# Performance work log

Measured on AMD Instinct MI355X. Metric: run time of the kernel, lower is better.

The kernel has to match this reference:

```python
import jax, jax.numpy as jnp
import numpy as np
from jax import lax

GRID_N = 80
C_FEAT = 128
HID = 256
NLAYERS = 12


def _make_grid_mesh(n):
    xs = np.linspace(-0.9, 0.9, n, dtype=np.float32)
    X, Y = np.meshgrid(xs, xs, indexing='xy')
    verts = np.stack([X.ravel(), Y.ravel(), np.zeros(n * n, np.float32)], 1)
    idx = np.arange(n * n).reshape(n, n)
    a = idx[:-1, :-1].ravel(); b = idx[:-1, 1:].ravel()
    c = idx[1:, :-1].ravel(); d = idx[1:, 1:].ravel()
    faces = np.concatenate([np.stack([a, b, c], 1), np.stack([b, d, c], 1)], 0)
    return verts, faces.astype(np.int64)


def _edges_and_inv(faces):
    F = faces.shape[0]
    e = np.concatenate([faces[:, [0, 1]], faces[:, [1, 2]], faces[:, [2, 0]]], 0)
    e = np.sort(e, 1)
    edges, inv = np.unique(e, axis=0, return_inverse=True)
    inv = inv.reshape(-1)
    return edges.astype(np.int32), inv[:F], inv[F:2 * F], inv[2 * F:]


def _subdivide_faces(faces, V):
    # new vertex k is midpoint of unique edge k, placed at index V + k
    edges, i01, i12, i20 = _edges_and_inv(faces)
    m01 = V + i01; m12 = V + i12; m20 = V + i20
    v0, v1, v2 = faces[:, 0], faces[:, 1], faces[:, 2]
    nf = np.concatenate([np.stack([v0, m01, m20], 1), np.stack([v1, m12, m01], 1),
                         np.stack([v2, m20, m12], 1), np.stack([m01, m12, m20], 1)], 0)
    return edges, nf


def _topology():
    verts0, f1 = _make_grid_mesh(GRID_N)
    V1 = verts0.shape[0]
    edges1, f2 = _subdivide_faces(f1, V1)
    V2 = V1 + edges1.shape[0]
    edges2, f3 = _subdivide_faces(f2, V2)
    V3 = V2 + edges2.shape[0]
    edges3 = _edges_and_inv(f3)[0]
    return verts0, edges1, edges2, edges3, V3


def _vert_align(feat, verts):
    # feat [C,H,W]; sample bilinearly at vertex (x,y) in [-1,1], align_corners, zero padding
    C, H, W = feat.shape
    fx = (verts[:, 0] + 1.0) * 0.5 * (W - 1)
    fy = (verts[:, 1] + 1.0) * 0.5 * (H - 1)
    x0 = jnp.floor(fx); y0 = jnp.floor(fy)
    wx = fx - x0; wy = fy - y0
    x0i = x0.astype(jnp.int32); y0i = y0.astype(jnp.int32)
    fT = jnp.transpose(feat, (1, 2, 0))  # [H,W,C]

    def samp(yi, xi):
        valid = ((yi >= 0) & (yi < H) & (xi >= 0) & (xi < W)).astype(feat.dtype)
        v = fT[jnp.clip(yi, 0, H - 1), jnp.clip(xi, 0, W - 1)]
        return v * valid[:, None]

    return (samp(y0i, x0i) * ((1 - wy) * (1 - wx))[:, None]
            + samp(y0i, x0i + 1) * ((1 - wy) * wx)[:, None]
            + samp(y0i + 1, x0i) * (wy * (1 - wx))[:, None]
            + samp(y0i + 1, x0i + 1) * (wy * wx)[:, None])


def _gconv(x, e0, e1, w, b):
    # pytorch3d GraphConv: w0(x) + sum_{j in N(i)} w1(x_j), undirected edges
    h0 = x @ w[0] + b[0]
    h1 = x @ w[1] + b[1]
    agg = jnp.zeros_like(h0).at[e0].add(h1[e1]).at[e1].add(h1[e0])
    return h0 + agg


def _stage(feat, edges, w_in, b_in, w_h, b_h, w_out, b_out):
    e0, e1 = edges[:, 0], edges[:, 1]
    x = _gconv(feat, e0, e1, w_in, b_in)

    def body(xc, p):
        return _gconv(xc, e0, e1, p[0], p[1]), None

    x, _ = lax.scan(body, x, (w_h, b_h))
    coords = _gconv(x, e0, e1, w_out, b_out)
    return x, coords


def _subdiv(f, edges):
    # SubdivideMeshes feature/vertex rule: append edge midpoints
    return jnp.concatenate([f, 0.5 * (f[edges[:, 0]] + f[edges[:, 1]])], 0)


def setup_inputs() -> dict:
    key = jax.random.key(0)
    ks = jax.random.split(key, 16)
    verts0, edges1, edges2, edges3, V3 = _topology()

    def pw(k, din, dout, L=None):
        shape = (L, 2, din, dout) if L else (2, din, dout)
        return jax.random.normal(k, shape, dtype=jnp.float32) / np.float32(np.sqrt(7.0 * din))

    din2 = C_FEAT + HID
    inp = {
        'conv64': jax.random.normal(ks[0], (C_FEAT, 56, 56), jnp.float32),
        'conv128': jax.random.normal(ks[1], (C_FEAT, 28, 28), jnp.float32),
        'conv256': jax.random.normal(ks[2], (C_FEAT, 14, 14), jnp.float32),
        'verts0': jnp.asarray(verts0),
        'edges1': jnp.asarray(edges1), 'edges2': jnp.asarray(edges2), 'edges3': jnp.asarray(edges3),
        'w_in1': pw(ks[3], C_FEAT, HID), 'b_in1': jnp.zeros((2, HID), jnp.float32),
        'w_h1': pw(ks[4], HID, HID, NLAYERS), 'b_h1': jnp.zeros((NLAYERS, 2, HID), jnp.float32),
        'w_out1': pw(ks[5], HID, 3), 'b_out1': jnp.zeros((2, 3), jnp.float32),
        'w_in2': pw(ks[6], din2, HID), 'b_in2': jnp.zeros((2, HID), jnp.float32),
        'w_h2': pw(ks[7], HID, HID, NLAYERS), 'b_h2': jnp.zeros((NLAYERS, 2, HID), jnp.float32),
        'w_out2': pw(ks[8], HID, 3), 'b_out2': jnp.zeros((2, 3), jnp.float32),
        'w_in3': pw(ks[9], din2, HID), 'b_in3': jnp.zeros((2, HID), jnp.float32),
        'w_h3': pw(ks[10], HID, HID, NLAYERS), 'b_h3': jnp.zeros((NLAYERS, 2, HID), jnp.float32),
        'w_out3': pw(ks[11], HID, 3), 'b_out3': jnp.zeros((2, 3), jnp.float32),
    }
    return inp


def reference(conv64, conv128, conv256, verts0,
              w_in1, b_in1, w_h1, b_h1, w_out1, b_out1,
              w_in2, b_in2, w_h2, b_h2, w_out2, b_out2,
              w_in3, b_in3, w_h3, b_h3, w_out3, b_out3,
              edges1, edges2, edges3):
    # stage 1: vert_align on conv64 + 14 graph convs -> coords
    x, c1 = _stage(_vert_align(conv64, verts0), edges1, w_in1, b_in1, w_h1, b_h1, w_out1, b_out1)
    v2 = _subdiv(c1, edges1)
    h2 = _subdiv(x, edges1)
    f2 = jnp.concatenate([_vert_align(conv128, v2), h2], 1)
    x, c2 = _stage(f2, edges2, w_in2, b_in2, w_h2, b_h2, w_out2, b_out2)
    v3 = _subdiv(c2, edges2)
    h3 = _subdiv(x, edges2)
    f3 = jnp.concatenate([_vert_align(conv256, v3), h3], 1)
    _, c3 = _stage(f3, edges3, w_in3, b_in3, w_h3, b_h3, w_out3, b_out3)
    return c3
```

## Files before the change

kernel.cpp:

```cpp
#include <hip/hip_runtime.h>
#include <utility>

#define HID 256

typedef __attribute__((ext_vector_type(8))) short bf16x8;
typedef __attribute__((ext_vector_type(4))) float f32x4;
typedef __attribute__((ext_vector_type(4))) unsigned short us4;
typedef __attribute__((ext_vector_type(8))) unsigned short us8;

constexpr size_t MAXN3 = 100489;
constexpr size_t MAXE3 = 300200;

constexpr size_t OFF_IN1 = 0;
constexpr size_t OFF_IN2 = OFF_IN1 + 2 * 256 * 128;
constexpr size_t OFF_IN3 = OFF_IN2 + 2 * 256 * 384;
constexpr size_t OFF_H1  = OFF_IN3 + 2 * 256 * 384;
constexpr size_t OFF_H2  = OFF_H1 + 24 * 256 * 256;
constexpr size_t OFF_H3  = OFF_H2 + 24 * 256 * 256;
constexpr size_t WT_TOTAL = OFF_H3 + 24 * 256 * 256;

__device__ __attribute__((aligned(16))) unsigned short g_Ah[MAXN3 * 256];
__device__ __attribute__((aligned(16))) unsigned short g_Al[MAXN3 * 256];
__device__ __attribute__((aligned(16))) unsigned short g_Bh[MAXN3 * 256];
__device__ __attribute__((aligned(16))) unsigned short g_Bl[MAXN3 * 256];
__device__ __attribute__((aligned(16))) unsigned short g_Gh[MAXN3 * 256];
__device__ __attribute__((aligned(16))) unsigned short g_Gl[MAXN3 * 256];
__device__ __attribute__((aligned(16))) unsigned short g_Dh[MAXN3 * 256];
__device__ __attribute__((aligned(16))) unsigned short g_Dl[MAXN3 * 256];
__device__ __attribute__((aligned(16))) unsigned short g_VAh[MAXN3 * 128];
__device__ __attribute__((aligned(16))) unsigned short g_VAl[MAXN3 * 128];
__device__ float g_C0[MAXN3 * 3];
__device__ float g_C2[MAXN3 * 3];
__device__ float g_Vv[MAXN3 * 3];
__device__ float g_T [56 * 56 * 128];
__device__ __attribute__((aligned(16))) unsigned short g_Wth[WT_TOTAL];
__device__ __attribute__((aligned(16))) unsigned short g_Wtl[WT_TOTAL];
__device__ int g_deg   [MAXN3];
__device__ int g_rowptr[MAXN3 + 1];
__device__ int g_cursor[MAXN3];
__device__ int g_adj   [2 * MAXE3];
__device__ int g_bsum  [128];

__device__ inline float b2f(unsigned short h) {
  return __uint_as_float((unsigned)h << 16);
}
__device__ inline void fsplit(float f, unsigned short& h, unsigned short& l) {
  unsigned u = __float_as_uint(f);
  h = (unsigned short)(u >> 16);
  float hf = __uint_as_float(u & 0xffff0000u);
  l = (unsigned short)(__float_as_uint(f - hf) >> 16);
}

#define GLOAD16(g, l)                                                       \
  __builtin_amdgcn_global_load_lds(                                        \
      (const __attribute__((address_space(1))) unsigned*)(const void*)(g), \
      (__attribute__((address_space(3))) unsigned*)(void*)(l), 16, 0, 0)

__global__ __launch_bounds__(256) void k_wtrans(const float* __restrict__ W,
                                                unsigned short* __restrict__ Oh,
                                                unsigned short* __restrict__ Ol,
                                                int K) {
  __shared__ float Ls[64][65];
  int ktb = blockIdx.x, cb = blockIdx.y, mat = blockIdx.z;
  int nktb = gridDim.x;
  const float* Wm = W + (size_t)mat * K * 256;
  int t = threadIdx.x;
#pragma unroll
  for (int i = 0; i < 16; ++i) {
    int idx = i * 256 + t;
    int kk = idx >> 6, cc = idx & 63;
    Ls[kk][cc] = Wm[(size_t)(ktb * 64 + kk) * 256 + cb * 64 + cc];
  }
  __syncthreads();
  size_t tb = ((size_t)(mat * 4 + cb) * nktb + ktb) * 4096;
#pragma unroll
  for (int i = 0; i < 2; ++i) {
    int c = t * 2 + i;
    int n = c >> 3, sp = c & 7;
    int kbase = (sp ^ (n & 7)) * 8;
    unsigned short hb[8], lb[8];
#pragma unroll
    for (int j = 0; j < 8; ++j) {
      float v = Ls[kbase + j][n];
      unsigned short hi, lo;
      fsplit(v, hi, lo);
      hb[j] = hi;
      lb[j] = lo;
    }
    *(us4*)(Oh + tb + c * 8)     = (us4){hb[0], hb[1], hb[2], hb[3]};
    *(us4*)(Oh + tb + c * 8 + 4) = (us4){hb[4], hb[5], hb[6], hb[7]};
    *(us4*)(Ol + tb + c * 8)     = (us4){lb[0], lb[1], lb[2], lb[3]};
    *(us4*)(Ol + tb + c * 8 + 4) = (us4){lb[4], lb[5], lb[6], lb[7]};
  }
}


__global__ __launch_bounds__(256) void k_count(const int* __restrict__ edges,
                                               int* __restrict__ deg, int E) {
  int e = blockIdx.x * blockDim.x + threadIdx.x;
  if (e >= E) return;
  atomicAdd(&deg[edges[2 * e + 0]], 1);
  atomicAdd(&deg[edges[2 * e + 1]], 1);
}

__global__ __launch_bounds__(256) void k_scan_part(const int* __restrict__ deg,
                                                   int* __restrict__ bsum, int N) {
  __shared__ int s[256];
  int t = threadIdx.x;
  int base = blockIdx.x * 1024 + t * 4;
  int v = 0;
#pragma unroll
  for (int i = 0; i < 4; ++i) {
    int idx = base + i;
    if (idx < N) v += deg[idx];
  }
  s[t] = v;
  __syncthreads();
  for (int off = 128; off > 0; off >>= 1) {
    if (t < off) s[t] += s[t + off];
    __syncthreads();
  }
  if (t == 0) bsum[blockIdx.x] = s[0];
}

__global__ __launch_bounds__(128) void k_scan_top(int* __restrict__ bsum, int nb) {
  __shared__ int s[128];
  int t = threadIdx.x;
  s[t] = (t < nb) ? bsum[t] : 0;
  __syncthreads();
  for (int off = 1; off < 128; off <<= 1) {
    int v = (t >= off) ? s[t - off] : 0;
    __syncthreads();
    s[t] += v;
    __syncthreads();
  }
  if (t < nb) bsum[t] = (t == 0) ? 0 : s[t - 1];
}

__global__ __launch_bounds__(256) void k_scan_write(const int* __restrict__ deg,
                                                    const int* __restrict__ bsum,
                                                    int* __restrict__ rowptr,
                                                    int* __restrict__ cursor, int N) {
  __shared__ int s[256];
  int t = threadIdx.x;
  int base = blockIdx.x * 1024;
  int d[4];
  int local = 0;
#pragma unroll
  for (int i = 0; i < 4; ++i) {
    int idx = base + t * 4 + i;
    d[i] = (idx < N) ? deg[idx] : 0;
    local += d[i];
  }
  s[t] = local;
  __syncthreads();
  for (int off = 1; off < 256; off <<= 1) {
    int v = (t >= off) ? s[t - off] : 0;
    __syncthreads();
    s[t] += v;
    __syncthreads();
  }
  int run = bsum[blockIdx.x] + s[t] - local;
#pragma unroll
  for (int i = 0; i < 4; ++i) {
    int idx = base + t * 4 + i;
    if (idx < N) {
      rowptr[idx] = run;
      cursor[idx] = run;
    }
    run += d[i];
  }
  if (blockIdx.x == gridDim.x - 1 && t == 255) rowptr[N] = run;
}

__global__ __launch_bounds__(256) void k_fill(const int* __restrict__ edges,
                                              int* __restrict__ cursor,
                                              int* __restrict__ adj, int E) {
  int e = blockIdx.x * blockDim.x + threadIdx.x;
  if (e >= E) return;
  int a = edges[2 * e + 0];
  int b = edges[2 * e + 1];
  adj[atomicAdd(&cursor[a], 1)] = b;
  adj[atomicAdd(&cursor[b], 1)] = a;
}


__global__ __launch_bounds__(128) void k_transpose(const float* __restrict__ in,
                                                   float* __restrict__ out, int HW) {
  int p = blockIdx.x;
  int c = threadIdx.x;
  if (p < HW) out[(size_t)p * 128 + c] = in[(size_t)c * HW + p];
}

__global__ __launch_bounds__(128) void k_vert_align(const float* __restrict__ fT,
                                                    const float* __restrict__ verts,
                                                    unsigned short* __restrict__ oh,
                                                    unsigned short* __restrict__ ol,
                                                    int N, int H, int W) {
  int v = blockIdx.x;
  if (v >= N) return;
  int c = threadIdx.x;
  float vx = verts[(size_t)v * 3 + 0];
  float vy = verts[(size_t)v * 3 + 1];
  float fx = (vx + 1.f) * 0.5f * (float)(W - 1);
  float fy = (vy + 1.f) * 0.5f * (float)(H - 1);
  float x0f = floorf(fx), y0f = floorf(fy);
  float wx = fx - x0f, wy = fy - y0f;
  int x0 = (int)x0f, y0 = (int)y0f;
  float acc = 0.f;
#pragma unroll
  for (int dy = 0; dy < 2; ++dy) {
#pragma unroll
    for (int dx = 0; dx < 2; ++dx) {
      int yi = y0 + dy, xi = x0 + dx;
      bool valid = (yi >= 0) && (yi < H) && (xi >= 0) && (xi < W);
      int yc = min(max(yi, 0), H - 1);
      int xc = min(max(xi, 0), W - 1);
      float val = fT[((size_t)yc * W + xc) * 128 + c];
      float wgt = (dy ? wy : 1.f - wy) * (dx ? wx : 1.f - wx);
      acc += valid ? val * wgt : 0.f;
    }
  }
  unsigned short h, l;
  fsplit(acc, h, l);
  oh[(size_t)v * 128 + c] = h;
  ol[(size_t)v * 128 + c] = l;
}

template <int CH>
__global__ __launch_bounds__(256) void k_gather(const int* __restrict__ rowptr,
                                                const int* __restrict__ adj,
                                                const unsigned short* __restrict__ Xh,
                                                const unsigned short* __restrict__ Xl,
                                                unsigned short* __restrict__ Gh,
                                                unsigned short* __restrict__ Gl, int N) {
  constexpr int TPV = CH / 8;
  int idx = blockIdx.x * blockDim.x + threadIdx.x;
  int v = idx / TPV;
  if (v >= N) return;
  int c = (idx % TPV) * 8;
  float a[8] = {};
  int lo = rowptr[v], hi = rowptr[v + 1];
  for (int i = lo; i < hi; ++i) {
    size_t base = (size_t)adj[i] * CH + c;
    us8 h = *(const us8*)(Xh + base);
    us8 l = *(const us8*)(Xl + base);
#pragma unroll
    for (int j = 0; j < 8; ++j) a[j] += b2f(h[j]) + b2f(l[j]);
  }
  us8 oh, ol;
#pragma unroll
  for (int j = 0; j < 8; ++j) {
    unsigned short hh, ll;
    fsplit(a[j], hh, ll);
    oh[j] = hh;
    ol[j] = ll;
  }
  *(us8*)(Gh + (size_t)v * CH + c) = oh;
  *(us8*)(Gl + (size_t)v * CH + c) = ol;
}

struct Panels {
  const unsigned short* ph[4];
  const unsigned short* pl[4];
  int ks[4];
  int ld[4];
};

#define SWZ(row, slot) (((row) * 64) + (((slot) ^ ((row) & 7)) << 3))

__global__ __launch_bounds__(512, 2) void k_layer(
    Panels pd, int Kmm,
    const unsigned short* __restrict__ w0h, const unsigned short* __restrict__ w0l,
    const unsigned short* __restrict__ w1h, const unsigned short* __restrict__ w1l,
    int Kw,
    const float* __restrict__ b0, const float* __restrict__ b1,
    const int* __restrict__ deg,
    unsigned short* __restrict__ Yh, unsigned short* __restrict__ Yl, int N) {
  __shared__ __attribute__((aligned(16))) unsigned short Xh_lds[2][128 * 64];
  __shared__ __attribute__((aligned(16))) unsigned short Xl_lds[2][128 * 64];
  __shared__ __attribute__((aligned(16))) unsigned short Wh_lds[2][2 * 4096];
  __shared__ __attribute__((aligned(16))) unsigned short Wl_lds[2][2 * 4096];
  int tid = threadIdx.x;
  int lane = tid & 63;
  int wid = tid >> 6;
  int wm = wid >> 2;
  int wn = wid & 3;

  int nrt = (N + 127) >> 7;
  int total = nrt * 2;
  int flat = blockIdx.x;
  int rowtile, colblk;
  if ((flat & ~15) + 16 <= total) {
    int sub = flat & 15;
    rowtile = (flat >> 4) * 8 + (sub & 7);
    colblk = sub >> 3;
  } else {
    rowtile = flat >> 1;
    colblk = flat & 1;
  }
  int row0 = rowtile * 128;
  int col0 = colblk * 128;
  int nktbw = Kw >> 6;

  f32x4 acc[4][2];
#pragma unroll
  for (int m = 0; m < 4; ++m)
#pragma unroll
    for (int n = 0; n < 2; ++n) acc[m][n] = (f32x4){0.f, 0.f, 0.f, 0.f};

  auto STAGE = [&](int buf, int kt) {
    int pi = (kt >= pd.ks[1]) + (kt >= pd.ks[2]) + (kt >= pd.ks[3]);
    const unsigned short* bph = pd.ph[pi];
    const unsigned short* bpl = pd.pl[pi];
    int ld = pd.ld[pi];
    int koff = kt - pd.ks[pi];
#pragma unroll
    for (int i = 0; i < 2; ++i) {
      int c = tid + i * 512;
      int row = c >> 3, slot = c & 7;
      int vg = min(row0 + row, N - 1);
      size_t so = (size_t)vg * ld + koff + ((slot ^ (row & 7)) << 3);
      GLOAD16(bph + so, &Xh_lds[buf][(size_t)c * 8]);
      GLOAD16(bpl + so, &Xl_lds[buf][(size_t)c * 8]);
    }
    int ktb = (kt < Kw) ? (kt >> 6) : ((kt - Kw) >> 6);
    const unsigned short* mh = (kt < Kw) ? w0h : w1h;
    const unsigned short* ml = (kt < Kw) ? w0l : w1l;
#pragma unroll
    for (int i = 0; i < 2; ++i) {
      int c = tid + i * 512;
      int half = c >> 9, ci = c & 511;
      size_t tb = ((size_t)((2 * colblk + half) * nktbw + ktb)) * 4096 + (size_t)ci * 8;
      GLOAD16(mh + tb, &Wh_lds[buf][half * 4096 + ci * 8]);
      GLOAD16(ml + tb, &Wl_lds[buf][half * 4096 + ci * 8]);
    }
  };

  auto COMPUTE = [&](int buf) {
#pragma unroll
    for (int ks = 0; ks < 2; ++ks) {
      int slot = ks * 4 + (lane >> 4);
      bf16x8 ah[4], al[4];
#pragma unroll
      for (int m = 0; m < 4; ++m) {
        int row = wm * 64 + m * 16 + (lane & 15);
        int off = SWZ(row, slot);
        ah[m] = *(const bf16x8*)&Xh_lds[buf][off];
        al[m] = *(const bf16x8*)&Xl_lds[buf][off];
      }
      bf16x8 bh[2], bl[2];
#pragma unroll
      for (int n = 0; n < 2; ++n) {
        int nr = wn * 32 + n * 16 + (lane & 15);
        int off = (nr >> 6) * 4096 + SWZ(nr & 63, slot);
        bh[n] = *(const bf16x8*)&Wh_lds[buf][off];
        bl[n] = *(const bf16x8*)&Wl_lds[buf][off];
      }
#pragma unroll
      for (int m = 0; m < 4; ++m)
#pragma unroll
        for (int n = 0; n < 2; ++n) {
          f32x4 c = acc[m][n];
          c = __builtin_amdgcn_mfma_f32_16x16x32_bf16(al[m], bh[n], c, 0, 0, 0);
          c = __builtin_amdgcn_mfma_f32_16x16x32_bf16(ah[m], bl[n], c, 0, 0, 0);
          c = __builtin_amdgcn_mfma_f32_16x16x32_bf16(ah[m], bh[n], c, 0, 0, 0);
          acc[m][n] = c;
        }
    }
  };

  int nt = Kmm >> 6;
  STAGE(0, 0);
  __syncthreads();
  int buf = 0;
  for (int t = 0; t < nt; ++t) {
    if (t + 1 < nt) STAGE(buf ^ 1, (t + 1) << 6);
    COMPUTE(buf);
    __syncthreads();
    buf ^= 1;
  }

#pragma unroll
  for (int m = 0; m < 4; ++m) {
    int rbase = row0 + wm * 64 + m * 16 + (lane >> 4) * 4;
    float dv[4];
#pragma unroll
    for (int r = 0; r < 4; ++r)
      dv[r] = (rbase + r < N) ? (float)deg[rbase + r] : 0.f;
#pragma unroll
    for (int n = 0; n < 2; ++n) {
      int col = col0 + wn * 32 + n * 16 + (lane & 15);
      float bb0 = b0[col], bb1 = b1[col];
      f32x4 v = acc[m][n];
#pragma unroll
      for (int r = 0; r < 4; ++r) {
        int row = rbase + r;
        if (row < N) {
          unsigned short h, l;
          fsplit(v[r] + bb0 + dv[r] * bb1, h, l);
          Yh[(size_t)row * HID + col] = h;
          Yl[(size_t)row * HID + col] = l;
        }
      }
    }
  }
}

__global__ __launch_bounds__(256) void k_rowdot6(const unsigned short* __restrict__ Xh,
                                                 const unsigned short* __restrict__ Xl,
                                                 const float* __restrict__ W,
                                                 const float* __restrict__ b,
                                                 float* __restrict__ Y0,
                                                 float* __restrict__ Y1, int N) {
  int gid = blockIdx.x * blockDim.x + threadIdx.x;
  int row = gid >> 6;
  int lane = threadIdx.x & 63;
  if (row >= N) return;
  size_t base = (size_t)row * HID + lane * 4;
  us4 hv = *(const us4*)(Xh + base);
  us4 lv = *(const us4*)(Xl + base);
  float s[6] = {0.f, 0.f, 0.f, 0.f, 0.f, 0.f};
#pragma unroll
  for (int k = 0; k < 4; ++k) {
    float x = b2f(hv[k]) + b2f(lv[k]);
    int kk = lane * 4 + k;
#pragma unroll
    for (int j = 0; j < 3; ++j) {
      s[j]     += x * W[kk * 3 + j];
      s[3 + j] += x * W[768 + kk * 3 + j];
    }
  }
#pragma unroll
  for (int off = 32; off > 0; off >>= 1)
#pragma unroll
    for (int j = 0; j < 6; ++j) s[j] += __shfl_down(s[j], off);
  if (lane == 0) {
#pragma unroll
    for (int j = 0; j < 3; ++j) {
      Y0[(size_t)row * 3 + j] = s[j] + b[j];
      Y1[(size_t)row * 3 + j] = s[3 + j] + b[3 + j];
    }
  }
}

__global__ __launch_bounds__(256) void k_scatter3(const int* __restrict__ edges,
                                                  const float* __restrict__ H,
                                                  float* __restrict__ OUT, int E) {
  int e = blockIdx.x * blockDim.x + threadIdx.x;
  if (e >= E) return;
  int a = edges[(size_t)e * 2 + 0];
  int b = edges[(size_t)e * 2 + 1];
#pragma unroll
  for (int k = 0; k < 3; ++k) {
    atomicAdd(&OUT[(size_t)a * 3 + k], H[(size_t)b * 3 + k]);
    atomicAdd(&OUT[(size_t)b * 3 + k], H[(size_t)a * 3 + k]);
  }
}

__global__ __launch_bounds__(256) void k_subdiv3(const float* __restrict__ c,
                                                 const int* __restrict__ edges,
                                                 float* __restrict__ v, int N, int E) {
  int i = blockIdx.x * blockDim.x + threadIdx.x;
  if (i >= N + E) return;
  if (i < N) {
#pragma unroll
    for (int k = 0; k < 3; ++k) v[(size_t)i * 3 + k] = c[(size_t)i * 3 + k];
  } else {
    int e = i - N;
    int a = edges[(size_t)e * 2 + 0];
    int b = edges[(size_t)e * 2 + 1];
#pragma unroll
    for (int k = 0; k < 3; ++k)
      v[(size_t)i * 3 + k] = 0.5f * (c[(size_t)a * 3 + k] + c[(size_t)b * 3 + k]);
  }
}

__global__ __launch_bounds__(256) void k_subdiv_feat(const unsigned short* __restrict__ xh,
                                                     const unsigned short* __restrict__ xl,
                                                     const int* __restrict__ edges,
                                                     unsigned short* __restrict__ oh,
                                                     unsigned short* __restrict__ ol,
                                                     int N, int E) {
  int idx = blockIdx.x * blockDim.x + threadIdx.x;
  int v = idx >> 5;
  if (v >= N + E) return;
  int c = (idx & 31) * 8;
  us8 rh, rl;
  if (v < N) {
    rh = *(const us8*)(xh + (size_t)v * HID + c);
    rl = *(const us8*)(xl + (size_t)v * HID + c);
  } else {
    int e = v - N;
    int a = edges[(size_t)e * 2 + 0];
    int b = edges[(size_t)e * 2 + 1];
    us8 ahv = *(const us8*)(xh + (size_t)a * HID + c);
    us8 alv = *(const us8*)(xl + (size_t)a * HID + c);
    us8 bhv = *(const us8*)(xh + (size_t)b * HID + c);
    us8 blv = *(const us8*)(xl + (size_t)b * HID + c);
#pragma unroll
    for (int j = 0; j < 8; ++j) {
      float f = 0.5f * ((b2f(ahv[j]) + b2f(alv[j])) + (b2f(bhv[j]) + b2f(blv[j])));
      unsigned short hh, ll;
      fsplit(f, hh, ll);
      rh[j] = hh;
      rl[j] = ll;
    }
  }
  *(us8*)(oh + (size_t)v * HID + c) = rh;
  *(us8*)(ol + (size_t)v * HID + c) = rl;
}


extern "C" void kernel_launch(void* const* d_in, const int* in_sizes, int n_in,
                              void* d_out, int out_size, void* d_ws, size_t ws_size,
                              hipStream_t stream) {
  const float* conv64  = (const float*)d_in[0];
  const float* conv128 = (const float*)d_in[1];
  const float* conv256 = (const float*)d_in[2];
  const float* verts0  = (const float*)d_in[3];
  const int*   edges1  = (const int*)d_in[4];
  const int*   edges2  = (const int*)d_in[5];
  const int*   edges3  = (const int*)d_in[6];
  const float* w_in1 = (const float*)d_in[7],  *b_in1 = (const float*)d_in[8];
  const float* w_h1  = (const float*)d_in[9],  *b_h1  = (const float*)d_in[10];
  const float* w_out1= (const float*)d_in[11], *b_out1= (const float*)d_in[12];
  const float* w_in2 = (const float*)d_in[13], *b_in2 = (const float*)d_in[14];
  const float* w_h2  = (const float*)d_in[15], *b_h2  = (const float*)d_in[16];
  const float* w_out2= (const float*)d_in[17], *b_out2= (const float*)d_in[18];
  const float* w_in3 = (const float*)d_in[19], *b_in3 = (const float*)d_in[20];
  const float* w_h3  = (const float*)d_in[21], *b_h3  = (const float*)d_in[22];
  const float* w_out3= (const float*)d_in[23], *b_out3= (const float*)d_in[24];

  const int N1 = in_sizes[3] / 3;
  const int E1 = in_sizes[4] / 2;
  const int E2 = in_sizes[5] / 2;
  const int E3 = in_sizes[6] / 2;
  const int N2 = N1 + E1;
  const int N3 = N2 + E2;
  if ((size_t)N3 > MAXN3 || (size_t)E3 > MAXE3) return;

  unsigned short *Ah, *Al, *Bh, *Bl, *Gh, *Gl, *Dh, *Dl, *VAh, *VAl;
  float *C0, *C2, *Vv, *T;
  unsigned short *Wth, *Wtl;
  int *deg, *rowptr, *cursor, *adj, *bsum;
  hipGetSymbolAddress((void**)&Ah,  HIP_SYMBOL(g_Ah));
  hipGetSymbolAddress((void**)&Al,  HIP_SYMBOL(g_Al));
  hipGetSymbolAddress((void**)&Bh,  HIP_SYMBOL(g_Bh));
  hipGetSymbolAddress((void**)&Bl,  HIP_SYMBOL(g_Bl));
  hipGetSymbolAddress((void**)&Gh,  HIP_SYMBOL(g_Gh));
  hipGetSymbolAddress((void**)&Gl,  HIP_SYMBOL(g_Gl));
  hipGetSymbolAddress((void**)&Dh,  HIP_SYMBOL(g_Dh));
  hipGetSymbolAddress((void**)&Dl,  HIP_SYMBOL(g_Dl));
  hipGetSymbolAddress((void**)&VAh, HIP_SYMBOL(g_VAh));
  hipGetSymbolAddress((void**)&VAl, HIP_SYMBOL(g_VAl));
  hipGetSymbolAddress((void**)&C0, HIP_SYMBOL(g_C0));
  hipGetSymbolAddress((void**)&C2, HIP_SYMBOL(g_C2));
  hipGetSymbolAddress((void**)&Vv, HIP_SYMBOL(g_Vv));
  hipGetSymbolAddress((void**)&T,  HIP_SYMBOL(g_T));
  hipGetSymbolAddress((void**)&Wth, HIP_SYMBOL(g_Wth));
  hipGetSymbolAddress((void**)&Wtl, HIP_SYMBOL(g_Wtl));
  hipGetSymbolAddress((void**)&deg,    HIP_SYMBOL(g_deg));
  hipGetSymbolAddress((void**)&rowptr, HIP_SYMBOL(g_rowptr));
  hipGetSymbolAddress((void**)&cursor, HIP_SYMBOL(g_cursor));
  hipGetSymbolAddress((void**)&adj,    HIP_SYMBOL(g_adj));
  hipGetSymbolAddress((void**)&bsum,   HIP_SYMBOL(g_bsum));

  k_wtrans<<<dim3(2, 4, 2),  256, 0, stream>>>(w_in1, Wth + OFF_IN1, Wtl + OFF_IN1, 128);
  k_wtrans<<<dim3(6, 4, 2),  256, 0, stream>>>(w_in2, Wth + OFF_IN2, Wtl + OFF_IN2, 384);
  k_wtrans<<<dim3(6, 4, 2),  256, 0, stream>>>(w_in3, Wth + OFF_IN3, Wtl + OFF_IN3, 384);
  k_wtrans<<<dim3(4, 4, 24), 256, 0, stream>>>(w_h1,  Wth + OFF_H1,  Wtl + OFF_H1,  256);
  k_wtrans<<<dim3(4, 4, 24), 256, 0, stream>>>(w_h2,  Wth + OFF_H2,  Wtl + OFF_H2,  256);
  k_wtrans<<<dim3(4, 4, 24), 256, 0, stream>>>(w_h3,  Wth + OFF_H3,  Wtl + OFF_H3,  256);

  const int BIG = 0x7fffffff;

  auto layerGrid = [](int N) { return dim3((unsigned)(((N + 127) / 128) * 2)); };

  auto build_csr = [&](const int* edges, int E, int N) {
    hipMemsetAsync(deg, 0, (size_t)N * sizeof(int), stream);
    k_count<<<(E + 255) / 256, 256, 0, stream>>>(edges, deg, E);
    int nb = (N + 1023) / 1024;
    k_scan_part<<<nb, 256, 0, stream>>>(deg, bsum, N);
    k_scan_top<<<1, 128, 0, stream>>>(bsum, nb);
    k_scan_write<<<nb, 256, 0, stream>>>(deg, bsum, rowptr, cursor, N);
    k_fill<<<(E + 255) / 256, 256, 0, stream>>>(edges, cursor, adj, E);
  };

  auto gconv_hidden = [&](size_t offH, const float* bh, int N) {
    unsigned short *Xh = Ah, *Xl = Al, *Yh = Bh, *Yl = Bl;
    for (int l = 0; l < 12; ++l) {
      const unsigned short* w0h = Wth + offH + (size_t)(2 * l + 0) * 65536;
      const unsigned short* w0l = Wtl + offH + (size_t)(2 * l + 0) * 65536;
      const unsigned short* w1h = Wth + offH + (size_t)(2 * l + 1) * 65536;
      const unsigned short* w1l = Wtl + offH + (size_t)(2 * l + 1) * 65536;
      const float* b0 = bh + (size_t)l * 2 * HID;
      const float* b1 = b0 + HID;
      k_gather<256><<<((size_t)N * 32 + 255) / 256, 256, 0, stream>>>(
          rowptr, adj, Xh, Xl, Gh, Gl, N);
      Panels pd = {{Xh, Gh, nullptr, nullptr}, {Xl, Gl, nullptr, nullptr},
                   {0, 256, BIG, BIG}, {256, 256, 0, 0}};
      k_layer<<<layerGrid(N), 512, 0, stream>>>(pd, 512, w0h, w0l, w1h, w1l, 256,
                                                b0, b1, deg, Yh, Yl, N);
      std::swap(Xh, Yh);
      std::swap(Xl, Yl);
    }
  };

  auto gconv_out = [&](const unsigned short* Xh, const unsigned short* Xl,
                       const float* wo, const float* bo,
                       float* Cdst, const int* edges, int E, int N) {
    k_rowdot6<<<((size_t)N * 64 + 255) / 256, 256, 0, stream>>>(Xh, Xl, wo, bo, Cdst, C2, N);
    k_scatter3<<<(E + 255) / 256, 256, 0, stream>>>(edges, C2, Cdst, E);
  };

  build_csr(edges1, E1, N1);
  k_transpose<<<56 * 56, 128, 0, stream>>>(conv64, T, 56 * 56);
  k_vert_align<<<N1, 128, 0, stream>>>(T, verts0, VAh, VAl, N1, 56, 56);
  k_gather<128><<<((size_t)N1 * 16 + 255) / 256, 256, 0, stream>>>(
      rowptr, adj, VAh, VAl, Gh, Gl, N1);
  {
    Panels pd = {{VAh, Gh, nullptr, nullptr}, {VAl, Gl, nullptr, nullptr},
                 {0, 128, BIG, BIG}, {128, 128, 0, 0}};
    k_layer<<<layerGrid(N1), 512, 0, stream>>>(pd, 256,
        Wth + OFF_IN1, Wtl + OFF_IN1, Wth + OFF_IN1 + 32768, Wtl + OFF_IN1 + 32768, 128,
        b_in1, b_in1 + HID, deg, Ah, Al, N1);
  }
  gconv_hidden(OFF_H1, b_h1, N1);
  gconv_out(Ah, Al, w_out1, b_out1, C0, edges1, E1, N1);
  k_subdiv3<<<(N2 + 255) / 256, 256, 0, stream>>>(C0, edges1, Vv, N1, E1);
  k_subdiv_feat<<<((size_t)N2 * 32 + 255) / 256, 256, 0, stream>>>(
      Ah, Al, edges1, Dh, Dl, N1, E1);

  build_csr(edges2, E2, N2);
  k_transpose<<<28 * 28, 128, 0, stream>>>(conv128, T, 28 * 28);
  k_vert_align<<<N2, 128, 0, stream>>>(T, Vv, VAh, VAl, N2, 28, 28);
  k_gather<128><<<((size_t)N2 * 16 + 255) / 256, 256, 0, stream>>>(
      rowptr, adj, VAh, VAl, Gh, Gl, N2);
  k_gather<256><<<((size_t)N2 * 32 + 255) / 256, 256, 0, stream>>>(
      rowptr, adj, Dh, Dl, Bh, Bl, N2);
  {
    const size_t m0 = OFF_IN2, m1 = OFF_IN2 + (size_t)256 * 384;
    Panels pd = {{VAh, Dh, Gh, Bh}, {VAl, Dl, Gl, Bl},
                 {0, 128, 384, 512}, {128, 256, 128, 256}};
    k_layer<<<layerGrid(N2), 512, 0, stream>>>(pd, 768,
        Wth + m0, Wtl + m0, Wth + m1, Wtl + m1, 384,
        b_in2, b_in2 + HID, deg, Ah, Al, N2);
  }
  gconv_hidden(OFF_H2, b_h2, N2);
  gconv_out(Ah, Al, w_out2, b_out2, C0, edges2, E2, N2);
  k_subdiv3<<<(N3 + 255) / 256, 256, 0, stream>>>(C0, edges2, Vv, N2, E2);
  k_subdiv_feat<<<((size_t)N3 * 32 + 255) / 256, 256, 0, stream>>>(
      Ah, Al, edges2, Dh, Dl, N2, E2);

  build_csr(edges3, E3, N3);
  k_transpose<<<14 * 14, 128, 0, stream>>>(conv256, T, 14 * 14);
  k_vert_align<<<N3, 128, 0, stream>>>(T, Vv, VAh, VAl, N3, 14, 14);
  k_gather<128><<<((size_t)N3 * 16 + 255) / 256, 256, 0, stream>>>(
      rowptr, adj, VAh, VAl, Gh, Gl, N3);
  k_gather<256><<<((size_t)N3 * 32 + 255) / 256, 256, 0, stream>>>(
      rowptr, adj, Dh, Dl, Bh, Bl, N3);
  {
    const size_t m0 = OFF_IN3, m1 = OFF_IN3 + (size_t)256 * 384;
    Panels pd = {{VAh, Dh, Gh, Bh}, {VAl, Dl, Gl, Bl},
                 {0, 128, 384, 512}, {128, 256, 128, 256}};
    k_layer<<<layerGrid(N3), 512, 0, stream>>>(pd, 768,
        Wth + m0, Wtl + m0, Wth + m1, Wtl + m1, 384,
        b_in3, b_in3 + HID, deg, Ah, Al, N3);
  }
  gconv_hidden(OFF_H3, b_h3, N3);
  float* OUT = (float*)d_out;
  k_rowdot6<<<((size_t)N3 * 64 + 255) / 256, 256, 0, stream>>>(
      Ah, Al, w_out3, b_out3, OUT, C2, N3);
  k_scatter3<<<(E3 + 255) / 256, 256, 0, stream>>>(edges3, C2, OUT, E3);
}
```

Baseline: 4.377 ms.

## Replace double-buffered LDS pipeline with single buffer to fit two blocks per CU

The layer GEMM kernel drops its two-stage LDS double buffer and now uses a single buffer. Each K tile is loaded, synchronized, computed and synchronized again. This halves shared memory per block, so more blocks can be resident per CU to hide memory latency. The cost is losing the overlap of the next tile's loads with the current tile's MFMA work, plus an extra barrier per iteration.

```diff
diff --git a/kernel.cpp b/kernel.cpp
--- a/kernel.cpp
+++ b/kernel.cpp
@@ -277,10 +277,10 @@
     const float* __restrict__ b0, const float* __restrict__ b1,
     const int* __restrict__ deg,
     unsigned short* __restrict__ Yh, unsigned short* __restrict__ Yl, int N) {
-  __shared__ __attribute__((aligned(16))) unsigned short Xh_lds[2][128 * 64];
-  __shared__ __attribute__((aligned(16))) unsigned short Xl_lds[2][128 * 64];
-  __shared__ __attribute__((aligned(16))) unsigned short Wh_lds[2][2 * 4096];
-  __shared__ __attribute__((aligned(16))) unsigned short Wl_lds[2][2 * 4096];
+  __shared__ __attribute__((aligned(16))) unsigned short Xh_lds[128 * 64];
+  __shared__ __attribute__((aligned(16))) unsigned short Xl_lds[128 * 64];
+  __shared__ __attribute__((aligned(16))) unsigned short Wh_lds[2 * 4096];
+  __shared__ __attribute__((aligned(16))) unsigned short Wl_lds[2 * 4096];
   int tid = threadIdx.x;
   int lane = tid & 63;
   int wid = tid >> 6;
@@ -309,7 +309,7 @@
 #pragma unroll
     for (int n = 0; n < 2; ++n) acc[m][n] = (f32x4){0.f, 0.f, 0.f, 0.f};
 
-  auto STAGE = [&](int buf, int kt) {
+  for (int kt = 0; kt < Kmm; kt += 64) {
     int pi = (kt >= pd.ks[1]) + (kt >= pd.ks[2]) + (kt >= pd.ks[3]);
     const unsigned short* bph = pd.ph[pi];
     const unsigned short* bpl = pd.pl[pi];
@@ -321,23 +321,23 @@
       int row = c >> 3, slot = c & 7;
       int vg = min(row0 + row, N - 1);
       size_t so = (size_t)vg * ld + koff + ((slot ^ (row & 7)) << 3);
-      GLOAD16(bph + so, &Xh_lds[buf][(size_t)c * 8]);
-      GLOAD16(bpl + so, &Xl_lds[buf][(size_t)c * 8]);
-    }
-    int ktb = (kt < Kw) ? (kt >> 6) : ((kt - Kw) >> 6);
-    const unsigned short* mh = (kt < Kw) ? w0h : w1h;
-    const unsigned short* ml = (kt < Kw) ? w0l : w1l;
-#pragma unroll
-    for (int i = 0; i < 2; ++i) {
-      int c = tid + i * 512;
-      int half = c >> 9, ci = c & 511;
-      size_t tb = ((size_t)((2 * colblk + half) * nktbw + ktb)) * 4096 + (size_t)ci * 8;
-      GLOAD16(mh + tb, &Wh_lds[buf][half * 4096 + ci * 8]);
-      GLOAD16(ml + tb, &Wl_lds[buf][half * 4096 + ci * 8]);
-    }
-  };
-
-  auto COMPUTE = [&](int buf) {
+      GLOAD16(bph + so, &Xh_lds[(size_t)c * 8]);
+      GLOAD16(bpl + so, &Xl_lds[(size_t)c * 8]);
+    }
+    {
+      int ktb = (kt < Kw) ? (kt >> 6) : ((kt - Kw) >> 6);
+      const unsigned short* mh = (kt < Kw) ? w0h : w1h;
+      const unsigned short* ml = (kt < Kw) ? w0l : w1l;
+#pragma unroll
+      for (int i = 0; i < 2; ++i) {
+        int c = tid + i * 512;
+        int half = c >> 9, ci = c & 511;
+        size_t tb = ((size_t)((2 * colblk + half) * nktbw + ktb)) * 4096 + (size_t)ci * 8;
+        GLOAD16(mh + tb, &Wh_lds[half * 4096 + ci * 8]);
+        GLOAD16(ml + tb, &Wl_lds[half * 4096 + ci * 8]);
+      }
+    }
+    __syncthreads();
 #pragma unroll
     for (int ks = 0; ks < 2; ++ks) {
       int slot = ks * 4 + (lane >> 4);
@@ -346,16 +346,16 @@
       for (int m = 0; m < 4; ++m) {
         int row = wm * 64 + m * 16 + (lane & 15);
         int off = SWZ(row, slot);
-        ah[m] = *(const bf16x8*)&Xh_lds[buf][off];
-        al[m] = *(const bf16x8*)&Xl_lds[buf][off];
+        ah[m] = *(const bf16x8*)&Xh_lds[off];
+        al[m] = *(const bf16x8*)&Xl_lds[off];
       }
       bf16x8 bh[2], bl[2];
 #pragma unroll
       for (int n = 0; n < 2; ++n) {
         int nr = wn * 32 + n * 16 + (lane & 15);
         int off = (nr >> 6) * 4096 + SWZ(nr & 63, slot);
-        bh[n] = *(const bf16x8*)&Wh_lds[buf][off];
-        bl[n] = *(const bf16x8*)&Wl_lds[buf][off];
+        bh[n] = *(const bf16x8*)&Wh_lds[off];
+        bl[n] = *(const bf16x8*)&Wl_lds[off];
       }
 #pragma unroll
       for (int m = 0; m < 4; ++m)
@@ -368,17 +368,7 @@
           acc[m][n] = c;
         }
     }
-  };
-
-  int nt = Kmm >> 6;
-  STAGE(0, 0);
-  __syncthreads();
-  int buf = 0;
-  for (int t = 0; t < nt; ++t) {
-    if (t + 1 < nt) STAGE(buf ^ 1, (t + 1) << 6);
-    COMPUTE(buf);
     __syncthreads();
-    buf ^= 1;
   }
 
 #pragma unroll
```

New measurement: 3.905 ms. 1.12x faster.
